# Kernel optimization log

Hardware: AMD Instinct MI355X
Metric: run time of the kernel (lower is better)

## Reference

```python
import jax, jax.numpy as jnp
import numpy as np

N, E, D = 100000, 1280000, 64


def setup_inputs() -> dict:
    key = jax.random.key(0)
    ks = jax.random.split(key, 9)
    x = jax.random.normal(ks[0], (N, D), jnp.float32)
    edge_index = jax.random.randint(ks[1], (2, E), 0, N, dtype=jnp.int64)
    edge_weight = jax.random.uniform(ks[2], (E,), jnp.float32)
    s = 1.0 / np.sqrt(D)
    W0 = jax.random.normal(ks[3], (D, D), jnp.float32) * s
    b0 = jnp.zeros((D,), jnp.float32)
    W1 = jax.random.normal(ks[4], (D, D), jnp.float32) * s
    b1 = jnp.zeros((D,), jnp.float32)
    W2 = jax.random.normal(ks[5], (D, D), jnp.float32) * s
    b2 = jnp.zeros((D,), jnp.float32)
    return {"x": x, "edge_index": edge_index, "edge_weight": edge_weight,
            "W0": W0, "b0": b0, "W1": W1, "b1": b1, "W2": W2, "b2": b2}


def reference(x, edge_index, edge_weight, W0, b0, W1, b1, W2, b2):
    n = x.shape[0]
    row, col = edge_index[0], edge_index[1]
    # GCN normalization with self-loops (PyG gcn_norm, fill_value=1)
    loop = jnp.arange(n)
    row_f = jnp.concatenate([row, loop])
    col_f = jnp.concatenate([col, loop])
    w_f = jnp.concatenate([edge_weight, jnp.ones((n,), x.dtype)])
    deg = jax.ops.segment_sum(w_f, col_f, num_segments=n)
    dinv = jnp.where(deg > 0, jax.lax.rsqrt(deg), 0.0).astype(x.dtype)
    norm = dinv[row_f] * w_f * dinv[col_f]  # [E+N]

    def conv(h, W, b):
        h = h @ W                                  # [N, D_out]
        msg = h[row_f] * norm[:, None]             # gather + scale
        return jax.ops.segment_sum(msg, col_f, num_segments=n) + b

    results = [x]
    h = jax.nn.relu(conv(x, W0, b0))   # dropout p=0 / eval -> identity
    results.append(h)
    h = jax.nn.relu(conv(h, W1, b1))
    results.append(h)
    h = conv(h, W2, b2)                # last layer: no activation
    results.append(h)
    return tuple(results)
```

## Files before the change

kernel.cpp:

```cpp
#include <hip/hip_runtime.h>
#include <hip/hip_fp16.h>


#define TPB 256
#define P1_CHUNK 4096
#define DSH 7
#define DNB 128
#define STAGE_CAP 4096

__global__ __launch_bounds__(TPB) void k_p0(const int* __restrict__ col,
                                            int* __restrict__ chist, int E, int nbk) {
    __shared__ int h[1024];
    int tid = threadIdx.x;
    for (int i = tid; i < nbk; i += TPB) h[i] = 0;
    __syncthreads();
    int s0 = blockIdx.x * P1_CHUNK;
    int s1 = min(s0 + P1_CHUNK, E);
    for (int i = s0 + tid; i < s1; i += TPB) atomicAdd(&h[col[i] >> DSH], 1);
    __syncthreads();
    for (int i = tid; i < nbk; i += TPB)
        if (h[i]) atomicAdd(&chist[i], h[i]);
}

__global__ __launch_bounds__(1024) void k_scanb(const int* __restrict__ chist,
                                                int* __restrict__ cbase,
                                                int* __restrict__ ccur, int nbk, int E) {
    __shared__ int s[1024];
    int tid = threadIdx.x;
    int v = (tid < nbk) ? chist[tid] : 0;
    s[tid] = v;
    __syncthreads();
    for (int off = 1; off < 1024; off <<= 1) {
        int t = (tid >= off) ? s[tid - off] : 0;
        __syncthreads();
        s[tid] += t;
        __syncthreads();
    }
    if (tid < nbk) { int ex = s[tid] - v; cbase[tid] = ex; ccur[tid] = ex; }
    if (tid == 0) cbase[nbk] = E;
}

__global__ __launch_bounds__(TPB) void k_p1(const int* __restrict__ row,
                                            const int* __restrict__ col,
                                            const float* __restrict__ w,
                                            int* __restrict__ ccur,
                                            int2* __restrict__ bkt, int E, int nbk) {
    __shared__ int h[1024];
    __shared__ int base[1024];
    int tid = threadIdx.x;
    for (int i = tid; i < nbk; i += TPB) h[i] = 0;
    __syncthreads();
    int s0 = blockIdx.x * P1_CHUNK;
    int s1 = min(s0 + P1_CHUNK, E);
    for (int i = s0 + tid; i < s1; i += TPB) atomicAdd(&h[col[i] >> DSH], 1);
    __syncthreads();
    for (int i = tid; i < nbk; i += TPB) {
        int c = h[i];
        base[i] = c ? atomicAdd(&ccur[i], c) : 0;
        h[i] = 0;
    }
    __syncthreads();
    for (int i = s0 + tid; i < s1; i += TPB) {
        int c = col[i];
        int b = c >> DSH;
        int r = atomicAdd(&h[b], 1);
        bkt[base[b] + r] = make_int2(row[i] | ((c & (DNB - 1)) << 20), __float_as_int(w[i]));
    }
}

__global__ __launch_bounds__(TPB) void k_p2(const int2* __restrict__ bkt,
                                            const int* __restrict__ cbase,
                                            int* __restrict__ starts,
                                            int2* __restrict__ edges,
                                            float* __restrict__ dinv, int n, int E) {
    __shared__ int hist[DNB];
    __shared__ int curs[DNB];
    __shared__ int sc[DNB];
    __shared__ int2 stage[STAGE_CAP];
    int tid = threadIdx.x;
    int b = blockIdx.x;
    int s0 = cbase[b], s1 = cbase[b + 1];
    int cnt = s1 - s0;
    int nodeBase = b << DSH;
    if (tid < DNB) hist[tid] = 0;
    __syncthreads();
    for (int i = s0 + tid; i < s1; i += TPB)
        atomicAdd(&hist[(unsigned)bkt[i].x >> 20], 1);
    __syncthreads();
    int v = 0;
    if (tid < DNB) { v = hist[tid]; sc[tid] = v; }
    __syncthreads();
    for (int off = 1; off < DNB; off <<= 1) {
        int t = 0;
        if (tid < DNB && tid >= off) t = sc[tid - off];
        __syncthreads();
        if (tid < DNB) sc[tid] += t;
        __syncthreads();
    }
    if (tid < DNB) {
        int ex = sc[tid] - v;
        curs[tid] = ex;
        int node = nodeBase + tid;
        if (node < n) starts[node] = s0 + ex;
    }
    if (b == 0 && tid == 0) starts[n] = E;
    __syncthreads();
    if (cnt <= STAGE_CAP) {
        for (int i = s0 + tid; i < s1; i += TPB) {
            int2 ed = bkt[i];
            int d = (unsigned)ed.x >> 20;
            int r = atomicAdd(&curs[d], 1);
            stage[r] = make_int2(ed.x & 0xFFFFF, ed.y);
        }
        __syncthreads();
        for (int i = tid; i < cnt; i += TPB) edges[s0 + i] = stage[i];
        if (tid < DNB) {
            int node = nodeBase + tid;
            if (node < n) {
                float d = 1.0f;
                for (int j = sc[tid] - v; j < sc[tid]; ++j)
                    d += __int_as_float(stage[j].y);
                dinv[node] = rsqrtf(d);
            }
        }
    } else {
        for (int i = s0 + tid; i < s1; i += TPB) {
            int2 ed = bkt[i];
            int d = (unsigned)ed.x >> 20;
            int r = atomicAdd(&curs[d], 1);
            edges[s0 + r] = make_int2(ed.x & 0xFFFFF, ed.y);
        }
        __syncthreads();
        if (tid < DNB) {
            int node = nodeBase + tid;
            if (node < n) {
                float d = 1.0f;
                for (int j = sc[tid] - v; j < sc[tid]; ++j)
                    d += __int_as_float(edges[s0 + j].y);
                dinv[node] = rsqrtf(d);
            }
        }
    }
}

__global__ __launch_bounds__(TPB, 3) void k_gemm64(const float* __restrict__ in,
                                                   const float* __restrict__ Wg,
                                                   __half* __restrict__ hwh,
                                                   const float* __restrict__ dinvg,
                                                   float* __restrict__ cp, int n) {
    __shared__ float4 Ws[1024];
    __shared__ float4 As[2048];
    int tid = threadIdx.x;
    const float4* Wf4 = (const float4*)Wg;
    #pragma unroll
    for (int i = 0; i < 4; ++i) Ws[i * 256 + tid] = Wf4[i * 256 + tid];
    int rowbase = blockIdx.x * 128;
    const float4* Af4 = (const float4*)in;
    #pragma unroll
    for (int i = 0; i < 8; ++i) {
        int f4 = i * 256 + tid;
        int r = f4 >> 4, c4 = f4 & 15;
        float4 v = make_float4(0.f, 0.f, 0.f, 0.f);
        if (rowbase + r < n) {
            v = Af4[(size_t)(rowbase + r) * 16 + c4];
            if (cp) *(float4*)&cp[((size_t)(rowbase + r) * 16 + c4) * 4] = v;
        }
        As[r * 16 + (c4 ^ ((r >> 3) & 3))] = v;
    }
    __syncthreads();
    int jg = tid & 15;
    int rg = tid >> 4;
    int r0 = rg * 8;
    int sw = rg & 3;
    float4 acc[8];
    #pragma unroll
    for (int rr = 0; rr < 8; ++rr) acc[rr] = make_float4(0.f, 0.f, 0.f, 0.f);
    #pragma unroll 2
    for (int kt = 0; kt < 16; ++kt) {
        float4 w0 = Ws[(kt * 4 + 0) * 16 + jg];
        float4 w1 = Ws[(kt * 4 + 1) * 16 + jg];
        float4 w2 = Ws[(kt * 4 + 2) * 16 + jg];
        float4 w3 = Ws[(kt * 4 + 3) * 16 + jg];
        int ac = kt ^ sw;
        #pragma unroll
        for (int rr = 0; rr < 8; ++rr) {
            float4 a = As[(r0 + rr) * 16 + ac];
            acc[rr].x = fmaf(a.x, w0.x, acc[rr].x);
            acc[rr].y = fmaf(a.x, w0.y, acc[rr].y);
            acc[rr].z = fmaf(a.x, w0.z, acc[rr].z);
            acc[rr].w = fmaf(a.x, w0.w, acc[rr].w);
            acc[rr].x = fmaf(a.y, w1.x, acc[rr].x);
            acc[rr].y = fmaf(a.y, w1.y, acc[rr].y);
            acc[rr].z = fmaf(a.y, w1.z, acc[rr].z);
            acc[rr].w = fmaf(a.y, w1.w, acc[rr].w);
            acc[rr].x = fmaf(a.z, w2.x, acc[rr].x);
            acc[rr].y = fmaf(a.z, w2.y, acc[rr].y);
            acc[rr].z = fmaf(a.z, w2.z, acc[rr].z);
            acc[rr].w = fmaf(a.z, w2.w, acc[rr].w);
            acc[rr].x = fmaf(a.w, w3.x, acc[rr].x);
            acc[rr].y = fmaf(a.w, w3.y, acc[rr].y);
            acc[rr].z = fmaf(a.w, w3.z, acc[rr].z);
            acc[rr].w = fmaf(a.w, w3.w, acc[rr].w);
        }
    }
    #pragma unroll
    for (int rr = 0; rr < 8; ++rr) {
        int r = rowbase + r0 + rr;
        if (r < n) {
            float di = dinvg[r];
            ushort4 s;
            s.x = __half_as_ushort(__float2half(acc[rr].x * di));
            s.y = __half_as_ushort(__float2half(acc[rr].y * di));
            s.z = __half_as_ushort(__float2half(acc[rr].z * di));
            s.w = __half_as_ushort(__float2half(acc[rr].w * di));
            *(ushort4*)&hwh[(size_t)r * 64 + jg * 4] = s;
        }
    }
}

__global__ __launch_bounds__(TPB) void k_gather(const int* __restrict__ starts,
                                                const int2* __restrict__ edges,
                                                const __half* __restrict__ hwh,
                                                const float* __restrict__ dinv,
                                                const float* __restrict__ b,
                                                float* __restrict__ out,
                                                int n, int relu) {
    int node = __builtin_amdgcn_readfirstlane(blockIdx.x * (TPB / 64) + (threadIdx.x >> 6));
    if (node >= n) return;
    int lane = threadIdx.x & 63;
    int s0 = starts[node], s1 = starts[node + 1];
    const long long* epk = (const long long*)edges;
    float acc = 0.f;
    int e = s0;
    for (; e + 8 <= s1; e += 8) {
        long long v0 = epk[e + 0];
        long long v1 = epk[e + 1];
        long long v2 = epk[e + 2];
        long long v3 = epk[e + 3];
        long long v4 = epk[e + 4];
        long long v5 = epk[e + 5];
        long long v6 = epk[e + 6];
        long long v7 = epk[e + 7];
        float h0 = __half2float(hwh[(size_t)(int)v0 * 64 + lane]);
        float h1 = __half2float(hwh[(size_t)(int)v1 * 64 + lane]);
        float h2 = __half2float(hwh[(size_t)(int)v2 * 64 + lane]);
        float h3 = __half2float(hwh[(size_t)(int)v3 * 64 + lane]);
        float h4 = __half2float(hwh[(size_t)(int)v4 * 64 + lane]);
        float h5 = __half2float(hwh[(size_t)(int)v5 * 64 + lane]);
        float h6 = __half2float(hwh[(size_t)(int)v6 * 64 + lane]);
        float h7 = __half2float(hwh[(size_t)(int)v7 * 64 + lane]);
        acc = fmaf(h0, __int_as_float((int)(v0 >> 32)), acc);
        acc = fmaf(h1, __int_as_float((int)(v1 >> 32)), acc);
        acc = fmaf(h2, __int_as_float((int)(v2 >> 32)), acc);
        acc = fmaf(h3, __int_as_float((int)(v3 >> 32)), acc);
        acc = fmaf(h4, __int_as_float((int)(v4 >> 32)), acc);
        acc = fmaf(h5, __int_as_float((int)(v5 >> 32)), acc);
        acc = fmaf(h6, __int_as_float((int)(v6 >> 32)), acc);
        acc = fmaf(h7, __int_as_float((int)(v7 >> 32)), acc);
    }
    if (e + 4 <= s1) {
        long long v0 = epk[e + 0];
        long long v1 = epk[e + 1];
        long long v2 = epk[e + 2];
        long long v3 = epk[e + 3];
        float h0 = __half2float(hwh[(size_t)(int)v0 * 64 + lane]);
        float h1 = __half2float(hwh[(size_t)(int)v1 * 64 + lane]);
        float h2 = __half2float(hwh[(size_t)(int)v2 * 64 + lane]);
        float h3 = __half2float(hwh[(size_t)(int)v3 * 64 + lane]);
        acc = fmaf(h0, __int_as_float((int)(v0 >> 32)), acc);
        acc = fmaf(h1, __int_as_float((int)(v1 >> 32)), acc);
        acc = fmaf(h2, __int_as_float((int)(v2 >> 32)), acc);
        acc = fmaf(h3, __int_as_float((int)(v3 >> 32)), acc);
        e += 4;
    }
    if (e + 2 <= s1) {
        long long v0 = epk[e + 0];
        long long v1 = epk[e + 1];
        float h0 = __half2float(hwh[(size_t)(int)v0 * 64 + lane]);
        float h1 = __half2float(hwh[(size_t)(int)v1 * 64 + lane]);
        acc = fmaf(h0, __int_as_float((int)(v0 >> 32)), acc);
        acc = fmaf(h1, __int_as_float((int)(v1 >> 32)), acc);
        e += 2;
    }
    if (e < s1) {
        long long v0 = epk[e];
        float h0 = __half2float(hwh[(size_t)(int)v0 * 64 + lane]);
        acc = fmaf(h0, __int_as_float((int)(v0 >> 32)), acc);
    }
    float di = dinv[node];
    float self = __half2float(hwh[(size_t)node * 64 + lane]);
    float o = fmaf(self + acc, di, b[lane]);
    if (relu) o = o > 0.f ? o : 0.f;
    out[(size_t)node * 64 + lane] = o;
}

extern "C" void kernel_launch(void* const* d_in, const int* in_sizes, int n_in,
                              void* d_out, int out_size, void* d_ws, size_t ws_size,
                              hipStream_t stream) {
    const float* x = (const float*)d_in[0];
    const int* ei = (const int*)d_in[1];
    const float* ew = (const float*)d_in[2];
    const float* Wl[3] = {(const float*)d_in[3], (const float*)d_in[5], (const float*)d_in[7]};
    const float* Bl[3] = {(const float*)d_in[4], (const float*)d_in[6], (const float*)d_in[8]};

    const int n = in_sizes[0] / 64;
    const int E = in_sizes[2];
    const int* row = ei;
    const int* col = ei + E;
    float* out = (float*)d_out;

    const int nbk = (n + DNB - 1) >> DSH;
    const int p1b = (E + P1_CHUNK - 1) / P1_CHUNK;

    char* ws = (char*)d_ws;
    size_t o = 0;
    float* dinv  = (float*)(ws + o);  o = (o + (size_t)n * 4 + 255) & ~(size_t)255;
    __half* hwh  = (__half*)(ws + o);
    int2*  bkt   = (int2*)(ws + o);
    {
        size_t hb = (size_t)n * 128, bb = (size_t)E * 8;
        o = (o + (hb > bb ? hb : bb) + 255) & ~(size_t)255;
    }
    int* starts  = (int*)(ws + o);    o = (o + (size_t)(n + 1) * 4 + 255) & ~(size_t)255;
    int* chist   = (int*)(ws + o);    o = (o + 1024 * 4 + 255) & ~(size_t)255;
    int* cbase   = (int*)(ws + o);    o = (o + 1025 * 4 + 255) & ~(size_t)255;
    int* ccur    = (int*)(ws + o);    o = (o + 1024 * 4 + 255) & ~(size_t)255;
    int2* edges  = (int2*)(ws + o);

    hipMemsetAsync(chist, 0, (size_t)nbk * 4, stream);
    k_p0<<<p1b, TPB, 0, stream>>>(col, chist, E, nbk);
    k_scanb<<<1, 1024, 0, stream>>>(chist, cbase, ccur, nbk, E);
    k_p1<<<p1b, TPB, 0, stream>>>(row, col, ew, ccur, bkt, E, nbk);
    k_p2<<<nbk, TPB, 0, stream>>>(bkt, cbase, starts, edges, dinv, n, E);

    const float* hin = x;
    for (int L = 0; L < 3; ++L) {
        float* oseg = out + (size_t)(L + 1) * n * 64;
        k_gemm64<<<(n + 127) / 128, TPB, 0, stream>>>(hin, Wl[L], hwh, dinv, L == 0 ? out : nullptr, n);
        k_gather<<<(n * 64 + TPB - 1) / TPB, TPB, 0, stream>>>(starts, edges, hwh, dinv, Bl[L], oseg, n, L < 2 ? 1 : 0);
        hin = oseg;
    }
}
```

Baseline: 368.8 us.

## Use fp16 MFMA for the dense 64x64 layer GEMM

Replaces the FP32 FMA outer-product GEMM with MFMA 16x16x32 f16 instructions. A and W are converted to fp16 in swizzled shared memory, and the dinv scaling is folded into the A rows before the multiply. Results are staged back through shared memory so the global stores are coalesced 16-byte writes, and the occupancy hint is raised. This lowers ALU cost and register pressure in the GEMM, but quantising the inputs to fp16 before the multiply adds rounding error beyond the old fp16 output storage.

```diff
diff --git a/kernel.cpp b/kernel.cpp
--- a/kernel.cpp
+++ b/kernel.cpp
@@ -7,6 +7,9 @@
 #define DSH 7
 #define DNB 128
 #define STAGE_CAP 4096
+
+typedef _Float16 half8 __attribute__((ext_vector_type(8)));
+typedef float f32x4 __attribute__((ext_vector_type(4)));
 
 __global__ __launch_bounds__(TPB) void k_p0(const int* __restrict__ col,
                                             int* __restrict__ chist, int E, int nbk) {
@@ -143,77 +146,104 @@
     }
 }
 
-__global__ __launch_bounds__(TPB, 3) void k_gemm64(const float* __restrict__ in,
+__global__ __launch_bounds__(TPB, 4) void k_gemm64(const float* __restrict__ in,
                                                    const float* __restrict__ Wg,
                                                    __half* __restrict__ hwh,
                                                    const float* __restrict__ dinvg,
                                                    float* __restrict__ cp, int n) {
-    __shared__ float4 Ws[1024];
-    __shared__ float4 As[2048];
-    int tid = threadIdx.x;
-    const float4* Wf4 = (const float4*)Wg;
+    __shared__ _Float16 As[128 * 64];
+    __shared__ _Float16 Bs[64 * 64];
+    int tid = threadIdx.x;
+    int rowbase = blockIdx.x * 128;
+
+    {
+        const float4* W4 = (const float4*)Wg;
+        #pragma unroll
+        for (int it = 0; it < 4; ++it) {
+            int k = (tid >> 4) + 16 * it;
+            int n0 = (tid & 15) * 4;
+            float4 wv = W4[k * 16 + (tid & 15)];
+            #pragma unroll
+            for (int j = 0; j < 4; ++j) {
+                int nn = n0 + j;
+                float e = (j == 0) ? wv.x : (j == 1) ? wv.y : (j == 2) ? wv.z : wv.w;
+                Bs[nn * 64 + (((k >> 3) ^ (nn & 7)) << 3) + (k & 7)] = (_Float16)e;
+            }
+        }
+    }
+    {
+        int r = tid >> 1;
+        int gr = rowbase + r;
+        int c0 = (tid & 1) * 32;
+        float di = (gr < n) ? dinvg[gr] : 0.f;
+        const float4* A4 = (const float4*)in;
+        #pragma unroll
+        for (int j = 0; j < 4; ++j) {
+            float4 v0 = make_float4(0.f, 0.f, 0.f, 0.f);
+            float4 v1 = v0;
+            if (gr < n) {
+                v0 = A4[(size_t)gr * 16 + (c0 >> 2) + j * 2];
+                v1 = A4[(size_t)gr * 16 + (c0 >> 2) + j * 2 + 1];
+                if (cp) {
+                    *(float4*)&cp[((size_t)gr * 16 + (c0 >> 2) + j * 2) * 4] = v0;
+                    *(float4*)&cp[((size_t)gr * 16 + (c0 >> 2) + j * 2 + 1) * 4] = v1;
+                }
+            }
+            int c4 = (c0 >> 3) + j;
+            half8 hv;
+            hv[0] = (_Float16)(v0.x * di); hv[1] = (_Float16)(v0.y * di);
+            hv[2] = (_Float16)(v0.z * di); hv[3] = (_Float16)(v0.w * di);
+            hv[4] = (_Float16)(v1.x * di); hv[5] = (_Float16)(v1.y * di);
+            hv[6] = (_Float16)(v1.z * di); hv[7] = (_Float16)(v1.w * di);
+            *(half8*)&As[r * 64 + ((c4 ^ (r & 7)) << 3)] = hv;
+        }
+    }
+    __syncthreads();
+
+    int w = tid >> 6;
+    int lane = tid & 63;
+    int l15 = lane & 15, l4 = lane >> 4;
+    f32x4 acc[2][4];
     #pragma unroll
-    for (int i = 0; i < 4; ++i) Ws[i * 256 + tid] = Wf4[i * 256 + tid];
-    int rowbase = blockIdx.x * 128;
-    const float4* Af4 = (const float4*)in;
+    for (int mt = 0; mt < 2; ++mt)
+        #pragma unroll
+        for (int nt = 0; nt < 4; ++nt) acc[mt][nt] = (f32x4){0.f, 0.f, 0.f, 0.f};
+    const half8* Av = (const half8*)As;
+    const half8* Bv = (const half8*)Bs;
     #pragma unroll
-    for (int i = 0; i < 8; ++i) {
-        int f4 = i * 256 + tid;
-        int r = f4 >> 4, c4 = f4 & 15;
-        float4 v = make_float4(0.f, 0.f, 0.f, 0.f);
-        if (rowbase + r < n) {
-            v = Af4[(size_t)(rowbase + r) * 16 + c4];
-            if (cp) *(float4*)&cp[((size_t)(rowbase + r) * 16 + c4) * 4] = v;
-        }
-        As[r * 16 + (c4 ^ ((r >> 3) & 3))] = v;
-    }
-    __syncthreads();
-    int jg = tid & 15;
-    int rg = tid >> 4;
-    int r0 = rg * 8;
-    int sw = rg & 3;
-    float4 acc[8];
+    for (int kk = 0; kk < 2; ++kk) {
+        int ck = kk * 4 + l4;
+        half8 a0 = Av[(w * 32 + l15) * 8 + (ck ^ (l15 & 7))];
+        half8 a1 = Av[(w * 32 + 16 + l15) * 8 + (ck ^ (l15 & 7))];
+        #pragma unroll
+        for (int nt = 0; nt < 4; ++nt) {
+            half8 b = Bv[(nt * 16 + l15) * 8 + (ck ^ (l15 & 7))];
+            acc[0][nt] = __builtin_amdgcn_mfma_f32_16x16x32_f16(a0, b, acc[0][nt], 0, 0, 0);
+            acc[1][nt] = __builtin_amdgcn_mfma_f32_16x16x32_f16(a1, b, acc[1][nt], 0, 0, 0);
+        }
+    }
+    __syncthreads();
+
     #pragma unroll
-    for (int rr = 0; rr < 8; ++rr) acc[rr] = make_float4(0.f, 0.f, 0.f, 0.f);
-    #pragma unroll 2
-    for (int kt = 0; kt < 16; ++kt) {
-        float4 w0 = Ws[(kt * 4 + 0) * 16 + jg];
-        float4 w1 = Ws[(kt * 4 + 1) * 16 + jg];
-        float4 w2 = Ws[(kt * 4 + 2) * 16 + jg];
-        float4 w3 = Ws[(kt * 4 + 3) * 16 + jg];
-        int ac = kt ^ sw;
-        #pragma unroll
-        for (int rr = 0; rr < 8; ++rr) {
-            float4 a = As[(r0 + rr) * 16 + ac];
-            acc[rr].x = fmaf(a.x, w0.x, acc[rr].x);
-            acc[rr].y = fmaf(a.x, w0.y, acc[rr].y);
-            acc[rr].z = fmaf(a.x, w0.z, acc[rr].z);
-            acc[rr].w = fmaf(a.x, w0.w, acc[rr].w);
-            acc[rr].x = fmaf(a.y, w1.x, acc[rr].x);
-            acc[rr].y = fmaf(a.y, w1.y, acc[rr].y);
-            acc[rr].z = fmaf(a.y, w1.z, acc[rr].z);
-            acc[rr].w = fmaf(a.y, w1.w, acc[rr].w);
-            acc[rr].x = fmaf(a.z, w2.x, acc[rr].x);
-            acc[rr].y = fmaf(a.z, w2.y, acc[rr].y);
-            acc[rr].z = fmaf(a.z, w2.z, acc[rr].z);
-            acc[rr].w = fmaf(a.z, w2.w, acc[rr].w);
-            acc[rr].x = fmaf(a.w, w3.x, acc[rr].x);
-            acc[rr].y = fmaf(a.w, w3.y, acc[rr].y);
-            acc[rr].z = fmaf(a.w, w3.z, acc[rr].z);
-            acc[rr].w = fmaf(a.w, w3.w, acc[rr].w);
-        }
-    }
+    for (int mt = 0; mt < 2; ++mt)
+        #pragma unroll
+        for (int nt = 0; nt < 4; ++nt)
+            #pragma unroll
+            for (int rg = 0; rg < 4; ++rg) {
+                int r = w * 32 + mt * 16 + l4 * 4 + rg;
+                int c = nt * 16 + l15;
+                As[r * 64 + (((c >> 3) ^ (r & 7)) << 3) + (c & 7)] =
+                    (_Float16)acc[mt][nt][rg];
+            }
+    __syncthreads();
     #pragma unroll
-    for (int rr = 0; rr < 8; ++rr) {
-        int r = rowbase + r0 + rr;
-        if (r < n) {
-            float di = dinvg[r];
-            ushort4 s;
-            s.x = __half_as_ushort(__float2half(acc[rr].x * di));
-            s.y = __half_as_ushort(__float2half(acc[rr].y * di));
-            s.z = __half_as_ushort(__float2half(acc[rr].z * di));
-            s.w = __half_as_ushort(__float2half(acc[rr].w * di));
-            *(ushort4*)&hwh[(size_t)r * 64 + jg * 4] = s;
+    for (int it = 0; it < 4; ++it) {
+        int idx = it * 256 + tid;
+        int r = idx >> 3, c4 = idx & 7;
+        int gr = rowbase + r;
+        if (gr < n) {
+            half8 hv = *(const half8*)&As[r * 64 + ((c4 ^ (r & 7)) << 3)];
+            *(half8*)&hwh[(size_t)gr * 64 + c4 * 8] = hv;
         }
     }
 }
```

Result: faster. 359.7 us (-2.5%).
